# Kernel tuning notes

Measured on AMD Instinct MI355X. Metric: run time of the kernel, lower is better.

## Reference

```python
import jax, jax.numpy as jnp
import numpy as np

N = 100000      # number of edge features (rows of feats)
M = 800000      # number of triplets
HID = 128
HEADS = 8
DH = HID // HEADS


def setup_inputs() -> dict:
    key = jax.random.key(0)
    ks = jax.random.split(key, 10)
    s = 1.0 / np.sqrt(HID)
    inp = {
        "feats": jax.random.normal(ks[0], (N, HID), dtype=jnp.float32),
        "idx_kj": jax.random.randint(ks[1], (M,), 0, N, dtype=jnp.int64),
        "idx_ji": jax.random.randint(ks[2], (M,), 0, N, dtype=jnp.int64),
        "Wv": jax.random.uniform(ks[3], (HID, HID), jnp.float32, -s, s),
        "Wq": jax.random.uniform(ks[4], (HID, HID), jnp.float32, -s, s),
        "Wk": jax.random.uniform(ks[5], (HID, HID), jnp.float32, -s, s),
        "W1": jax.random.uniform(ks[6], (HID, HID), jnp.float32, -s, s),
        "b1": jax.random.uniform(ks[7], (HID,), jnp.float32, -s, s),
        "W2": jax.random.uniform(ks[8], (HID, HID), jnp.float32, -s, s),
        "b2": jax.random.uniform(ks[9], (HID,), jnp.float32, -s, s),
    }
    return inp


def reference(feats, idx_kj, idx_ji, Wv, Wq, Wk, W1, b1, W2, b2):
    # Projections (no bias), reshape to [N, H, Dh]
    v = (feats @ Wv.T).reshape(N, HEADS, DH)
    k = (feats @ Wk.T).reshape(N, HEADS, DH)
    q = (feats @ Wq.T).reshape(N, HEADS, DH)

    # edge-indexed attention scores: [M, H, 1]
    att = jnp.sum(q[idx_kj] * k[idx_ji], axis=-1, keepdims=True)
    att = jnp.exp(jax.nn.leaky_relu(att, negative_slope=0.2))  # unsafe softmax, as in source

    # segment-sum normalizer over destination index idx_ji: [N, H, 1]
    denom = jax.ops.segment_sum(att, idx_ji, num_segments=N)
    att = att / denom[idx_ji]

    # weighted V gather-scatter: [M, HID] -> [N, HID]
    v_att = (v[idx_kj] * att).reshape(M, HID)
    agg = jax.ops.segment_sum(v_att, idx_ji, num_segments=N)  # v_clone after +scatter-v

    v_flat = v.reshape(N, HID)
    # ResidualLayer (dropout in eval mode -> identity): v + relu(lin2(relu(lin1(agg))))
    h = jax.nn.relu(agg @ W1.T + b1)
    h = jax.nn.relu(h @ W2.T + b2)
    return v_flat + h
```

## Files before the change

kernel.cpp:

```cpp
#include <hip/hip_runtime.h>
#include <hip/hip_bf16.h>
#include <math.h>

#define N_NODES 100000
#define M_EDGES 800000
#define HID 128
#define HEADS 8
#define DH 16
#define SCAN_NB ((N_NODES + 1023) / 1024)

typedef __attribute__((ext_vector_type(8))) short short8;
typedef __attribute__((ext_vector_type(4))) float floatx4;

__device__ __forceinline__ ushort f32_to_bf16(float x) {
    __hip_bfloat16 h = __float2bfloat16(x);
    union { __hip_bfloat16 h; ushort u; } c; c.h = h;
    return c.u;
}
__device__ __forceinline__ float bf16_bits_to_f32(ushort u) {
    union { unsigned int i; float f; } c; c.i = ((unsigned int)u) << 16;
    return c.f;
}
__device__ __forceinline__ float bf16pair_lo(unsigned int p) {
    union { unsigned int i; float f; } c; c.i = p << 16; return c.f;
}
__device__ __forceinline__ float bf16pair_hi(unsigned int p) {
    union { unsigned int i; float f; } c; c.i = p & 0xffff0000u; return c.f;
}

__device__ __forceinline__ void stage_w_frag(const ushort* __restrict__ W,
                                             ushort* __restrict__ lds, int tid)
{
    #pragma unroll
    for (int i = 0; i < 8; ++i) {
        int idx  = i * 256 + tid;
        int f    = idx >> 6;
        int lane = idx & 63;
        int t    = f & 7, ks = f >> 3;
        int row  = t * 16 + (lane & 15);
        int col  = ks * 32 + (lane >> 4) * 8;
        uint4 d = *(const uint4*)(W + row * HID + col);
        *(uint4*)(lds + idx * 8) = d;
    }
}

__global__ __launch_bounds__(256) void cvt_w_kernel(
    const float* __restrict__ Wq, const float* __restrict__ Wk, const float* __restrict__ Wv,
    const float* __restrict__ W1, const float* __restrict__ W2,
    ushort* __restrict__ dq, ushort* __restrict__ dk, ushort* __restrict__ dv,
    ushort* __restrict__ d1, ushort* __restrict__ d2)
{
    int i = blockIdx.x * 256 + threadIdx.x;
    int w = i >> 14;
    int j = i & 16383;
    const float* s[5] = {Wq, Wk, Wv, W1, W2};
    ushort*      d[5] = {dq, dk, dv, d1, d2};
    d[w][j] = f32_to_bf16(s[w][j]);
}

__global__ __launch_bounds__(256) void qkv_mfma_kernel(
    const float* __restrict__ feats,
    const ushort* __restrict__ Wq16, const ushort* __restrict__ Wk16, const ushort* __restrict__ Wv16,
    ushort* __restrict__ qv16, ushort* __restrict__ k16)
{
    __shared__ ushort wlds[16384];
    const int tid  = threadIdx.x;
    const int wave = tid >> 6;
    const int lane = tid & 63;
    const int row0 = blockIdx.x * 128 + wave * 32;
    const int lrow = lane & 15;
    const int lk   = (lane >> 4) * 8;
    const int crow = (lane >> 4) * 4;

    short8 afrag[2][4];
    bool tvalid[2];
    #pragma unroll
    for (int r = 0; r < 2; ++r) {
        int rr = row0 + r * 16;
        tvalid[r] = (rr < N_NODES);
        const float* arow = feats + (size_t)((tvalid[r] ? rr : 0) + lrow) * HID + lk;
        #pragma unroll
        for (int ks = 0; ks < 4; ++ks) {
            float4 f0 = *(const float4*)(arow + ks * 32);
            float4 f1 = *(const float4*)(arow + ks * 32 + 4);
            short8 a;
            a[0] = (short)f32_to_bf16(f0.x); a[1] = (short)f32_to_bf16(f0.y);
            a[2] = (short)f32_to_bf16(f0.z); a[3] = (short)f32_to_bf16(f0.w);
            a[4] = (short)f32_to_bf16(f1.x); a[5] = (short)f32_to_bf16(f1.y);
            a[6] = (short)f32_to_bf16(f1.z); a[7] = (short)f32_to_bf16(f1.w);
            afrag[r][ks] = a;
        }
    }

    const ushort* Ws[3] = {Wq16, Wk16, Wv16};
    ushort* Ob[3]; int Ostride[3];
    Ob[0] = qv16;       Ostride[0] = 256;
    Ob[1] = k16;        Ostride[1] = 128;
    Ob[2] = qv16 + 128; Ostride[2] = 256;

    #pragma unroll
    for (int w = 0; w < 3; ++w) {
        __syncthreads();
        stage_w_frag(Ws[w], wlds, tid);
        __syncthreads();

        floatx4 acc[2][8];
        #pragma unroll
        for (int r = 0; r < 2; ++r)
            #pragma unroll
            for (int t = 0; t < 8; ++t) acc[r][t] = (floatx4)(0.f);

        #pragma unroll
        for (int ks = 0; ks < 4; ++ks) {
            short8 B[8];
            #pragma unroll
            for (int t = 0; t < 8; ++t)
                B[t] = *(const short8*)&wlds[(ks * 8 + t) * 512 + lane * 8];
            #pragma unroll
            for (int t = 0; t < 8; ++t) {
                acc[0][t] = __builtin_amdgcn_mfma_f32_16x16x32_bf16(B[t], afrag[0][ks], acc[0][t], 0, 0, 0);
                acc[1][t] = __builtin_amdgcn_mfma_f32_16x16x32_bf16(B[t], afrag[1][ks], acc[1][t], 0, 0, 0);
            }
        }

        #pragma unroll
        for (int r = 0; r < 2; ++r) {
            if (tvalid[r]) {
                ushort* O = Ob[w] + (size_t)(row0 + r * 16 + lrow) * Ostride[w];
                #pragma unroll
                for (int t = 0; t < 8; ++t) {
                    ushort4 o;
                    o.x = f32_to_bf16(acc[r][t][0]); o.y = f32_to_bf16(acc[r][t][1]);
                    o.z = f32_to_bf16(acc[r][t][2]); o.w = f32_to_bf16(acc[r][t][3]);
                    *(ushort4*)(O + t * 16 + crow) = o;
                }
            }
        }
    }
}

__global__ __launch_bounds__(256) void hist_kernel(
    const int* __restrict__ idx_ji, int* __restrict__ count)
{
    int m = blockIdx.x * 256 + threadIdx.x;
    if (m < M_EDGES) atomicAdd(&count[idx_ji[m]], 1);
}

__global__ __launch_bounds__(256) void scan_blocksum_kernel(
    const int* __restrict__ count, int* __restrict__ blocksum)
{
    __shared__ int s[256];
    const int tid = threadIdx.x;
    const int base = blockIdx.x * 1024 + tid * 4;
    int sum = 0;
    if (base + 3 < N_NODES) {
        int4 c = *(const int4*)(count + base);
        sum = c.x + c.y + c.z + c.w;
    } else {
        #pragma unroll
        for (int j = 0; j < 4; ++j) if (base + j < N_NODES) sum += count[base + j];
    }
    s[tid] = sum;
    __syncthreads();
    for (int off = 128; off > 0; off >>= 1) {
        if (tid < off) s[tid] += s[tid + off];
        __syncthreads();
    }
    if (tid == 0) blocksum[blockIdx.x] = s[0];
}

__global__ __launch_bounds__(128) void scan_top_kernel(int* __restrict__ blocksum)
{
    __shared__ int s[128];
    const int t = threadIdx.x;
    int v = (t < SCAN_NB) ? blocksum[t] : 0;
    s[t] = v;
    __syncthreads();
    for (int off = 1; off < 128; off <<= 1) {
        int x = (t >= off) ? s[t - off] : 0;
        __syncthreads();
        s[t] += x;
        __syncthreads();
    }
    if (t < SCAN_NB) blocksum[t] = s[t] - v;
}

__global__ __launch_bounds__(256) void scan_write_kernel(
    const int* __restrict__ count, const int* __restrict__ blocksum,
    int* __restrict__ offsets, int* __restrict__ cursor)
{
    __shared__ int s[256];
    const int tid = threadIdx.x;
    const int base = blockIdx.x * 1024 + tid * 4;
    int c0 = 0, c1 = 0, c2 = 0, c3 = 0;
    if (base + 3 < N_NODES) {
        int4 c = *(const int4*)(count + base);
        c0 = c.x; c1 = c.y; c2 = c.z; c3 = c.w;
    } else {
        if (base     < N_NODES) c0 = count[base];
        if (base + 1 < N_NODES) c1 = count[base + 1];
        if (base + 2 < N_NODES) c2 = count[base + 2];
        if (base + 3 < N_NODES) c3 = count[base + 3];
    }
    const int tsum = c0 + c1 + c2 + c3;
    s[tid] = tsum;
    __syncthreads();
    for (int off = 1; off < 256; off <<= 1) {
        int x = (tid >= off) ? s[tid - off] : 0;
        __syncthreads();
        s[tid] += x;
        __syncthreads();
    }
    int o0 = s[tid] - tsum + blocksum[blockIdx.x];
    int o1 = o0 + c0, o2 = o1 + c1, o3 = o2 + c2;
    if (base + 3 < N_NODES) {
        *(int4*)(offsets + base) = make_int4(o0, o1, o2, o3);
        *(int4*)(cursor  + base) = make_int4(o0, o1, o2, o3);
    } else {
        if (base     < N_NODES) { offsets[base]     = o0; cursor[base]     = o0; }
        if (base + 1 < N_NODES) { offsets[base + 1] = o1; cursor[base + 1] = o1; }
        if (base + 2 < N_NODES) { offsets[base + 2] = o2; cursor[base + 2] = o2; }
        if (base + 3 < N_NODES) { offsets[base + 3] = o3; cursor[base + 3] = o3; }
    }
}

__global__ __launch_bounds__(256) void fill_kernel(
    const int* __restrict__ idx_ji, const int* __restrict__ idx_kj,
    int* __restrict__ cursor, int* __restrict__ edge_kj)
{
    int m = blockIdx.x * 256 + threadIdx.x;
    if (m < M_EDGES) {
        int pos = atomicAdd(&cursor[idx_ji[m]], 1);
        edge_kj[pos] = idx_kj[m];
    }
}

__global__ __launch_bounds__(256) void aggregate_kernel(
    const int* __restrict__ edge_kj, const int* __restrict__ offsets,
    const int* __restrict__ count, const ushort* __restrict__ qv16,
    const ushort* __restrict__ k16, ushort* __restrict__ agg16)
{
    const int gid  = blockIdx.x * 256 + threadIdx.x;
    const int node = gid >> 4;
    const int l16  = threadIdx.x & 15;
    if (node >= N_NODES) return;

    const int deg  = count[node];
    const int base = offsets[node];

    float kn[8];
    {
        uint4 kp = *(const uint4*)(k16 + (size_t)node * HID + l16 * 8);
        const unsigned int* kw = (const unsigned int*)&kp;
        #pragma unroll
        for (int j = 0; j < 4; ++j) {
            kn[2*j]   = bf16pair_lo(kw[j]);
            kn[2*j+1] = bf16pair_hi(kw[j]);
        }
    }

    float acc[8] = {0.f,0.f,0.f,0.f,0.f,0.f,0.f,0.f};
    float d = 0.f;

    int e = 0;
    for (; e + 2 <= deg; e += 2) {
        const int kj0 = edge_kj[base + e];
        const int kj1 = edge_kj[base + e + 1];
        const ushort* r0 = qv16 + (size_t)kj0 * 256 + l16 * 8;
        const ushort* r1 = qv16 + (size_t)kj1 * 256 + l16 * 8;
        uint4 qp0 = *(const uint4*)r0;
        uint4 vp0 = *(const uint4*)(r0 + 128);
        uint4 qp1 = *(const uint4*)r1;
        uint4 vp1 = *(const uint4*)(r1 + 128);

        const unsigned int* q0 = (const unsigned int*)&qp0;
        const unsigned int* q1 = (const unsigned int*)&qp1;
        float p0 = 0.f, p1 = 0.f;
        #pragma unroll
        for (int j = 0; j < 4; ++j) {
            p0 += bf16pair_lo(q0[j]) * kn[2*j] + bf16pair_hi(q0[j]) * kn[2*j+1];
            p1 += bf16pair_lo(q1[j]) * kn[2*j] + bf16pair_hi(q1[j]) * kn[2*j+1];
        }
        p0 += __shfl_xor(p0, 1);
        p1 += __shfl_xor(p1, 1);
        float lr0 = (p0 >= 0.f) ? p0 : 0.2f * p0;
        float lr1 = (p1 >= 0.f) ? p1 : 0.2f * p1;
        float s0 = __expf(lr0);
        float s1 = __expf(lr1);
        d += s0 + s1;
        const unsigned int* v0 = (const unsigned int*)&vp0;
        const unsigned int* v1 = (const unsigned int*)&vp1;
        #pragma unroll
        for (int j = 0; j < 4; ++j) {
            acc[2*j]   += s0 * bf16pair_lo(v0[j]) + s1 * bf16pair_lo(v1[j]);
            acc[2*j+1] += s0 * bf16pair_hi(v0[j]) + s1 * bf16pair_hi(v1[j]);
        }
    }
    if (e < deg) {
        const int kj0 = edge_kj[base + e];
        const ushort* r0 = qv16 + (size_t)kj0 * 256 + l16 * 8;
        uint4 qp0 = *(const uint4*)r0;
        uint4 vp0 = *(const uint4*)(r0 + 128);
        const unsigned int* q0 = (const unsigned int*)&qp0;
        float p0 = 0.f;
        #pragma unroll
        for (int j = 0; j < 4; ++j)
            p0 += bf16pair_lo(q0[j]) * kn[2*j] + bf16pair_hi(q0[j]) * kn[2*j+1];
        p0 += __shfl_xor(p0, 1);
        float lr0 = (p0 >= 0.f) ? p0 : 0.2f * p0;
        float s0 = __expf(lr0);
        d += s0;
        const unsigned int* v0 = (const unsigned int*)&vp0;
        #pragma unroll
        for (int j = 0; j < 4; ++j) {
            acc[2*j]   += s0 * bf16pair_lo(v0[j]);
            acc[2*j+1] += s0 * bf16pair_hi(v0[j]);
        }
    }

    const float inv = (deg > 0) ? 1.f / d : 0.f;
    uint4 o;
    unsigned int* ow = (unsigned int*)&o;
    #pragma unroll
    for (int j = 0; j < 4; ++j)
        ow[j] = (unsigned int)f32_to_bf16(acc[2*j] * inv)
              | ((unsigned int)f32_to_bf16(acc[2*j+1] * inv) << 16);
    *(uint4*)(agg16 + (size_t)node * HID + l16 * 8) = o;
}

__global__ __launch_bounds__(256) void mlp_mfma_kernel(
    const ushort* __restrict__ agg16, const ushort* __restrict__ qv16,
    const ushort* __restrict__ W1_16, const float* __restrict__ b1,
    const ushort* __restrict__ W2_16, const float* __restrict__ b2,
    float* __restrict__ out)
{
    __shared__ ushort wlds[16384];
    __shared__ ushort h1s[16384];
    const int tid  = threadIdx.x;
    const int wave = tid >> 6;
    const int lane = tid & 63;
    const int row0 = blockIdx.x * 128 + wave * 32;
    const int lrow = lane & 15;
    const int lk   = (lane >> 4) * 8;
    const int crow = (lane >> 4) * 4;

    short8 afrag[2][4];
    bool tvalid[2];
    #pragma unroll
    for (int r = 0; r < 2; ++r) {
        int rr = row0 + r * 16;
        tvalid[r] = (rr < N_NODES);
        const ushort* arow = agg16 + (size_t)((tvalid[r] ? rr : 0) + lrow) * HID + lk;
        #pragma unroll
        for (int ks = 0; ks < 4; ++ks)
            afrag[r][ks] = *(const short8*)(arow + ks * 32);
    }

    stage_w_frag(W1_16, wlds, tid);
    __syncthreads();

    {
        floatx4 acc[2][8];
        #pragma unroll
        for (int r = 0; r < 2; ++r)
            #pragma unroll
            for (int t = 0; t < 8; ++t) acc[r][t] = (floatx4)(0.f);
        #pragma unroll
        for (int ks = 0; ks < 4; ++ks) {
            short8 B[8];
            #pragma unroll
            for (int t = 0; t < 8; ++t)
                B[t] = *(const short8*)&wlds[(ks * 8 + t) * 512 + lane * 8];
            #pragma unroll
            for (int t = 0; t < 8; ++t) {
                acc[0][t] = __builtin_amdgcn_mfma_f32_16x16x32_bf16(B[t], afrag[0][ks], acc[0][t], 0, 0, 0);
                acc[1][t] = __builtin_amdgcn_mfma_f32_16x16x32_bf16(B[t], afrag[1][ks], acc[1][t], 0, 0, 0);
            }
        }
        #pragma unroll
        for (int r = 0; r < 2; ++r) {
            ushort* tile = &h1s[(wave * 2 + r) * 2048];
            #pragma unroll
            for (int t = 0; t < 8; ++t) {
                float4 bias = *(const float4*)(b1 + t * 16 + crow);
                ushort4 o;
                o.x = f32_to_bf16(fmaxf(acc[r][t][0] + bias.x, 0.f));
                o.y = f32_to_bf16(fmaxf(acc[r][t][1] + bias.y, 0.f));
                o.z = f32_to_bf16(fmaxf(acc[r][t][2] + bias.z, 0.f));
                o.w = f32_to_bf16(fmaxf(acc[r][t][3] + bias.w, 0.f));
                int ks   = t >> 1;
                int quad = (t & 1) * 2 + (crow >> 3);
                int j0   = crow & 4;
                *(ushort4*)(tile + (ks * 64 + quad * 16 + lrow) * 8 + j0) = o;
            }
        }
    }
    __syncthreads();
    stage_w_frag(W2_16, wlds, tid);
    __syncthreads();

    {
        short8 hfrag[2][4];
        #pragma unroll
        for (int r = 0; r < 2; ++r) {
            const ushort* tile = &h1s[(wave * 2 + r) * 2048];
            #pragma unroll
            for (int ks = 0; ks < 4; ++ks)
                hfrag[r][ks] = *(const short8*)(tile + (ks * 64 + lane) * 8);
        }
        floatx4 acc[2][8];
        #pragma unroll
        for (int r = 0; r < 2; ++r)
            #pragma unroll
            for (int t = 0; t < 8; ++t) acc[r][t] = (floatx4)(0.f);
        #pragma unroll
        for (int ks = 0; ks < 4; ++ks) {
            short8 B[8];
            #pragma unroll
            for (int t = 0; t < 8; ++t)
                B[t] = *(const short8*)&wlds[(ks * 8 + t) * 512 + lane * 8];
            #pragma unroll
            for (int t = 0; t < 8; ++t) {
                acc[0][t] = __builtin_amdgcn_mfma_f32_16x16x32_bf16(B[t], hfrag[0][ks], acc[0][t], 0, 0, 0);
                acc[1][t] = __builtin_amdgcn_mfma_f32_16x16x32_bf16(B[t], hfrag[1][ks], acc[1][t], 0, 0, 0);
            }
        }
        #pragma unroll
        for (int r = 0; r < 2; ++r) {
            if (tvalid[r]) {
                const size_t nrow = (size_t)(row0 + r * 16 + lrow);
                const ushort* vrow = qv16 + nrow * 256 + 128;
                float* orow = out + nrow * HID;
                #pragma unroll
                for (int t = 0; t < 8; ++t) {
                    float4 bias = *(const float4*)(b2 + t * 16 + crow);
                    ushort4 vv = *(const ushort4*)(vrow + t * 16 + crow);
                    float4 o;
                    o.x = bf16_bits_to_f32(vv.x) + fmaxf(acc[r][t][0] + bias.x, 0.f);
                    o.y = bf16_bits_to_f32(vv.y) + fmaxf(acc[r][t][1] + bias.y, 0.f);
                    o.z = bf16_bits_to_f32(vv.z) + fmaxf(acc[r][t][2] + bias.z, 0.f);
                    o.w = bf16_bits_to_f32(vv.w) + fmaxf(acc[r][t][3] + bias.w, 0.f);
                    *(float4*)(orow + t * 16 + crow) = o;
                }
            }
        }
    }
}

extern "C" void kernel_launch(void* const* d_in, const int* in_sizes, int n_in,
                              void* d_out, int out_size, void* d_ws, size_t ws_size,
                              hipStream_t stream) {
    const float* feats  = (const float*)d_in[0];
    const int*   idx_kj = (const int*)d_in[1];
    const int*   idx_ji = (const int*)d_in[2];
    const float* Wv     = (const float*)d_in[3];
    const float* Wq     = (const float*)d_in[4];
    const float* Wk     = (const float*)d_in[5];
    const float* W1     = (const float*)d_in[6];
    const float* b1     = (const float*)d_in[7];
    const float* W2     = (const float*)d_in[8];
    const float* b2     = (const float*)d_in[9];
    float* out = (float*)d_out;

    ushort* qv16    = (ushort*)d_ws;
    ushort* k16     = qv16    + (size_t)N_NODES * 256;
    ushort* agg16   = k16     + (size_t)N_NODES * HID;
    ushort* Wq16    = agg16   + (size_t)N_NODES * HID;
    ushort* Wk16    = Wq16 + HID * HID;
    ushort* Wv16    = Wk16 + HID * HID;
    ushort* W116    = Wv16 + HID * HID;
    ushort* W216    = W116 + HID * HID;
    int* count      = (int*)(W216 + HID * HID);
    int* offsets    = count + N_NODES;
    int* cursor     = offsets + N_NODES;
    int* blocksum   = cursor + N_NODES;
    int* edge_kj    = blocksum + ((SCAN_NB + 3) & ~3);

    hipMemsetAsync(count, 0, N_NODES * sizeof(int), stream);

    cvt_w_kernel<<<(5 * HID * HID + 255) / 256, 256, 0, stream>>>(
        Wq, Wk, Wv, W1, W2, Wq16, Wk16, Wv16, W116, W216);

    qkv_mfma_kernel<<<(N_NODES + 127) / 128, 256, 0, stream>>>(
        feats, Wq16, Wk16, Wv16, qv16, k16);

    hist_kernel<<<(M_EDGES + 255) / 256, 256, 0, stream>>>(idx_ji, count);
    scan_blocksum_kernel<<<SCAN_NB, 256, 0, stream>>>(count, blocksum);
    scan_top_kernel<<<1, 128, 0, stream>>>(blocksum);
    scan_write_kernel<<<SCAN_NB, 256, 0, stream>>>(count, blocksum, offsets, cursor);
    fill_kernel<<<(M_EDGES + 255) / 256, 256, 0, stream>>>(idx_ji, idx_kj, cursor, edge_kj);

    aggregate_kernel<<<((size_t)N_NODES * 16 + 255) / 256, 256, 0, stream>>>(
        edge_kj, offsets, count, qv16, k16, agg16);

    mlp_mfma_kernel<<<(N_NODES + 127) / 128, 256, 0, stream>>>(
        agg16, qv16, W116, b1, W216, b2, out);
}
```

Before: 328.5 us.

## Fold weight conversion, memset and top scan into kernels; pad CSR for vector edge loads

Removes the separate weight-conversion kernel by converting fp32 weights to bf16 while staging them into LDS. The count memset moves into the QKV kernel and the single-block top-level scan is recomputed redundantly in each scan_write block, which removes several launches. Per-node edge lists are padded to multiples of four so the aggregate loop can read four edge indices with one int4 load and issue four gathers per iteration. In exchange it adds redundant fp32 weight loads per block, a larger edge buffer, and wasted lanes on padded edges.

```diff
diff --git a/kernel.cpp b/kernel.cpp
--- a/kernel.cpp
+++ b/kernel.cpp
@@ -28,8 +28,8 @@
     union { unsigned int i; float f; } c; c.i = p & 0xffff0000u; return c.f;
 }
 
-__device__ __forceinline__ void stage_w_frag(const ushort* __restrict__ W,
-                                             ushort* __restrict__ lds, int tid)
+__device__ __forceinline__ void stage_w_frag_f32(const float* __restrict__ W,
+                                                 ushort* __restrict__ lds, int tid)
 {
     #pragma unroll
     for (int i = 0; i < 8; ++i) {
@@ -39,29 +39,23 @@
         int t    = f & 7, ks = f >> 3;
         int row  = t * 16 + (lane & 15);
         int col  = ks * 32 + (lane >> 4) * 8;
-        uint4 d = *(const uint4*)(W + row * HID + col);
-        *(uint4*)(lds + idx * 8) = d;
-    }
-}
-
-__global__ __launch_bounds__(256) void cvt_w_kernel(
-    const float* __restrict__ Wq, const float* __restrict__ Wk, const float* __restrict__ Wv,
-    const float* __restrict__ W1, const float* __restrict__ W2,
-    ushort* __restrict__ dq, ushort* __restrict__ dk, ushort* __restrict__ dv,
-    ushort* __restrict__ d1, ushort* __restrict__ d2)
-{
-    int i = blockIdx.x * 256 + threadIdx.x;
-    int w = i >> 14;
-    int j = i & 16383;
-    const float* s[5] = {Wq, Wk, Wv, W1, W2};
-    ushort*      d[5] = {dq, dk, dv, d1, d2};
-    d[w][j] = f32_to_bf16(s[w][j]);
+        const float* src = W + row * HID + col;
+        float4 a = *(const float4*)src;
+        float4 b = *(const float4*)(src + 4);
+        ushort4 lo, hi;
+        lo.x = f32_to_bf16(a.x); lo.y = f32_to_bf16(a.y);
+        lo.z = f32_to_bf16(a.z); lo.w = f32_to_bf16(a.w);
+        hi.x = f32_to_bf16(b.x); hi.y = f32_to_bf16(b.y);
+        hi.z = f32_to_bf16(b.z); hi.w = f32_to_bf16(b.w);
+        *(ushort4*)(lds + idx * 8)     = lo;
+        *(ushort4*)(lds + idx * 8 + 4) = hi;
+    }
 }
 
 __global__ __launch_bounds__(256) void qkv_mfma_kernel(
     const float* __restrict__ feats,
-    const ushort* __restrict__ Wq16, const ushort* __restrict__ Wk16, const ushort* __restrict__ Wv16,
-    ushort* __restrict__ qv16, ushort* __restrict__ k16)
+    const float* __restrict__ Wq, const float* __restrict__ Wk, const float* __restrict__ Wv,
+    ushort* __restrict__ qv16, ushort* __restrict__ k16, int* __restrict__ count)
 {
     __shared__ ushort wlds[16384];
     const int tid  = threadIdx.x;
@@ -71,6 +65,9 @@
     const int lrow = lane & 15;
     const int lk   = (lane >> 4) * 8;
     const int crow = (lane >> 4) * 4;
+
+    int z = blockIdx.x * 256 + tid;
+    if (z < N_NODES) count[z] = 0;
 
     short8 afrag[2][4];
     bool tvalid[2];
@@ -92,7 +89,7 @@
         }
     }
 
-    const ushort* Ws[3] = {Wq16, Wk16, Wv16};
+    const float* Ws[3] = {Wq, Wk, Wv};
     ushort* Ob[3]; int Ostride[3];
     Ob[0] = qv16;       Ostride[0] = 256;
     Ob[1] = k16;        Ostride[1] = 128;
@@ -101,7 +98,7 @@
     #pragma unroll
     for (int w = 0; w < 3; ++w) {
         __syncthreads();
-        stage_w_frag(Ws[w], wlds, tid);
+        stage_w_frag_f32(Ws[w], wlds, tid);
         __syncthreads();
 
         floatx4 acc[2][8];
@@ -155,10 +152,11 @@
     int sum = 0;
     if (base + 3 < N_NODES) {
         int4 c = *(const int4*)(count + base);
-        sum = c.x + c.y + c.z + c.w;
+        sum = ((c.x + 3) & ~3) + ((c.y + 3) & ~3) + ((c.z + 3) & ~3) + ((c.w + 3) & ~3);
     } else {
         #pragma unroll
-        for (int j = 0; j < 4; ++j) if (base + j < N_NODES) sum += count[base + j];
+        for (int j = 0; j < 4; ++j)
+            if (base + j < N_NODES) sum += (count[base + j] + 3) & ~3;
     }
     s[tid] = sum;
     __syncthreads();
@@ -167,22 +165,6 @@
         __syncthreads();
     }
     if (tid == 0) blocksum[blockIdx.x] = s[0];
-}
-
-__global__ __launch_bounds__(128) void scan_top_kernel(int* __restrict__ blocksum)
-{
-    __shared__ int s[128];
-    const int t = threadIdx.x;
-    int v = (t < SCAN_NB) ? blocksum[t] : 0;
-    s[t] = v;
-    __syncthreads();
-    for (int off = 1; off < 128; off <<= 1) {
-        int x = (t >= off) ? s[t - off] : 0;
-        __syncthreads();
-        s[t] += x;
-        __syncthreads();
-    }
-    if (t < SCAN_NB) blocksum[t] = s[t] - v;
 }
 
 __global__ __launch_bounds__(256) void scan_write_kernel(
@@ -190,17 +172,29 @@
     int* __restrict__ offsets, int* __restrict__ cursor)
 {
     __shared__ int s[256];
+    __shared__ int bs[128];
     const int tid = threadIdx.x;
+
+    if (tid < 128) bs[tid] = (tid < SCAN_NB) ? blocksum[tid] : 0;
+    __syncthreads();
+    for (int off = 1; off < 128; off <<= 1) {
+        int x = (tid >= off && tid < 128) ? bs[tid - off] : 0;
+        __syncthreads();
+        if (tid < 128) bs[tid] += x;
+        __syncthreads();
+    }
+    const int blockbase = (blockIdx.x == 0) ? 0 : bs[blockIdx.x - 1];
+
     const int base = blockIdx.x * 1024 + tid * 4;
     int c0 = 0, c1 = 0, c2 = 0, c3 = 0;
     if (base + 3 < N_NODES) {
         int4 c = *(const int4*)(count + base);
-        c0 = c.x; c1 = c.y; c2 = c.z; c3 = c.w;
+        c0 = (c.x + 3) & ~3; c1 = (c.y + 3) & ~3; c2 = (c.z + 3) & ~3; c3 = (c.w + 3) & ~3;
     } else {
-        if (base     < N_NODES) c0 = count[base];
-        if (base + 1 < N_NODES) c1 = count[base + 1];
-        if (base + 2 < N_NODES) c2 = count[base + 2];
-        if (base + 3 < N_NODES) c3 = count[base + 3];
+        if (base     < N_NODES) c0 = (count[base]     + 3) & ~3;
+        if (base + 1 < N_NODES) c1 = (count[base + 1] + 3) & ~3;
+        if (base + 2 < N_NODES) c2 = (count[base + 2] + 3) & ~3;
+        if (base + 3 < N_NODES) c3 = (count[base + 3] + 3) & ~3;
     }
     const int tsum = c0 + c1 + c2 + c3;
     s[tid] = tsum;
@@ -211,7 +205,7 @@
         s[tid] += x;
         __syncthreads();
     }
-    int o0 = s[tid] - tsum + blocksum[blockIdx.x];
+    int o0 = s[tid] - tsum + blockbase;
     int o1 = o0 + c0, o2 = o1 + c1, o3 = o2 + c2;
     if (base + 3 < N_NODES) {
         *(int4*)(offsets + base) = make_int4(o0, o1, o2, o3);
@@ -262,59 +256,47 @@
     float acc[8] = {0.f,0.f,0.f,0.f,0.f,0.f,0.f,0.f};
     float d = 0.f;
 
-    int e = 0;
-    for (; e + 2 <= deg; e += 2) {
-        const int kj0 = edge_kj[base + e];
-        const int kj1 = edge_kj[base + e + 1];
-        const ushort* r0 = qv16 + (size_t)kj0 * 256 + l16 * 8;
-        const ushort* r1 = qv16 + (size_t)kj1 * 256 + l16 * 8;
-        uint4 qp0 = *(const uint4*)r0;
-        uint4 vp0 = *(const uint4*)(r0 + 128);
-        uint4 qp1 = *(const uint4*)r1;
-        uint4 vp1 = *(const uint4*)(r1 + 128);
-
-        const unsigned int* q0 = (const unsigned int*)&qp0;
-        const unsigned int* q1 = (const unsigned int*)&qp1;
-        float p0 = 0.f, p1 = 0.f;
-        #pragma unroll
-        for (int j = 0; j < 4; ++j) {
-            p0 += bf16pair_lo(q0[j]) * kn[2*j] + bf16pair_hi(q0[j]) * kn[2*j+1];
-            p1 += bf16pair_lo(q1[j]) * kn[2*j] + bf16pair_hi(q1[j]) * kn[2*j+1];
-        }
-        p0 += __shfl_xor(p0, 1);
-        p1 += __shfl_xor(p1, 1);
-        float lr0 = (p0 >= 0.f) ? p0 : 0.2f * p0;
-        float lr1 = (p1 >= 0.f) ? p1 : 0.2f * p1;
-        float s0 = __expf(lr0);
-        float s1 = __expf(lr1);
-        d += s0 + s1;
-        const unsigned int* v0 = (const unsigned int*)&vp0;
-        const unsigned int* v1 = (const unsigned int*)&vp1;
-        #pragma unroll
-        for (int j = 0; j < 4; ++j) {
-            acc[2*j]   += s0 * bf16pair_lo(v0[j]) + s1 * bf16pair_lo(v1[j]);
-            acc[2*j+1] += s0 * bf16pair_hi(v0[j]) + s1 * bf16pair_hi(v1[j]);
-        }
-    }
-    if (e < deg) {
-        const int kj0 = edge_kj[base + e];
-        const ushort* r0 = qv16 + (size_t)kj0 * 256 + l16 * 8;
-        uint4 qp0 = *(const uint4*)r0;
-        uint4 vp0 = *(const uint4*)(r0 + 128);
-        const unsigned int* q0 = (const unsigned int*)&qp0;
-        float p0 = 0.f;
-        #pragma unroll
-        for (int j = 0; j < 4; ++j)
-            p0 += bf16pair_lo(q0[j]) * kn[2*j] + bf16pair_hi(q0[j]) * kn[2*j+1];
-        p0 += __shfl_xor(p0, 1);
-        float lr0 = (p0 >= 0.f) ? p0 : 0.2f * p0;
-        float s0 = __expf(lr0);
-        d += s0;
-        const unsigned int* v0 = (const unsigned int*)&vp0;
-        #pragma unroll
-        for (int j = 0; j < 4; ++j) {
-            acc[2*j]   += s0 * bf16pair_lo(v0[j]);
-            acc[2*j+1] += s0 * bf16pair_hi(v0[j]);
+    for (int e = 0; e < deg; e += 4) {
+        const int rem = deg - e;
+        int4 kj4 = *(const int4*)(edge_kj + base + e);
+        int kj[4];
+        kj[0] = kj4.x;
+        kj[1] = (rem > 1) ? kj4.y : kj4.x;
+        kj[2] = (rem > 2) ? kj4.z : kj4.x;
+        kj[3] = (rem > 3) ? kj4.w : kj4.x;
+
+        uint4 qp[4], vp[4];
+        #pragma unroll
+        for (int i = 0; i < 4; ++i) {
+            const ushort* r = qv16 + (size_t)kj[i] * 256 + l16 * 8;
+            qp[i] = *(const uint4*)r;
+            vp[i] = *(const uint4*)(r + 128);
+        }
+
+        float p[4];
+        #pragma unroll
+        for (int i = 0; i < 4; ++i) {
+            const unsigned int* q = (const unsigned int*)&qp[i];
+            float x = 0.f;
+            #pragma unroll
+            for (int j = 0; j < 4; ++j)
+                x += bf16pair_lo(q[j]) * kn[2*j] + bf16pair_hi(q[j]) * kn[2*j+1];
+            p[i] = x;
+        }
+        #pragma unroll
+        for (int i = 0; i < 4; ++i) p[i] += __shfl_xor(p[i], 1);
+
+        #pragma unroll
+        for (int i = 0; i < 4; ++i) {
+            float lr = (p[i] >= 0.f) ? p[i] : 0.2f * p[i];
+            float s  = (i < rem) ? __expf(lr) : 0.f;
+            d += s;
+            const unsigned int* v = (const unsigned int*)&vp[i];
+            #pragma unroll
+            for (int j = 0; j < 4; ++j) {
+                acc[2*j]   += s * bf16pair_lo(v[j]);
+                acc[2*j+1] += s * bf16pair_hi(v[j]);
+            }
         }
     }
 
@@ -330,8 +312,8 @@
 
 __global__ __launch_bounds__(256) void mlp_mfma_kernel(
     const ushort* __restrict__ agg16, const ushort* __restrict__ qv16,
-    const ushort* __restrict__ W1_16, const float* __restrict__ b1,
-    const ushort* __restrict__ W2_16, const float* __restrict__ b2,
+    const float* __restrict__ W1, const float* __restrict__ b1,
+    const float* __restrict__ W2, const float* __restrict__ b2,
     float* __restrict__ out)
 {
     __shared__ ushort wlds[16384];
@@ -356,7 +338,7 @@
             afrag[r][ks] = *(const short8*)(arow + ks * 32);
     }
 
-    stage_w_frag(W1_16, wlds, tid);
+    stage_w_frag_f32(W1, wlds, tid);
     __syncthreads();
 
     {
@@ -396,7 +378,7 @@
         }
     }
     __syncthreads();
-    stage_w_frag(W2_16, wlds, tid);
+    stage_w_frag_f32(W2, wlds, tid);
     __syncthreads();
 
     {
@@ -465,28 +447,17 @@
     ushort* qv16    = (ushort*)d_ws;
     ushort* k16     = qv16    + (size_t)N_NODES * 256;
     ushort* agg16   = k16     + (size_t)N_NODES * HID;
-    ushort* Wq16    = agg16   + (size_t)N_NODES * HID;
-    ushort* Wk16    = Wq16 + HID * HID;
-    ushort* Wv16    = Wk16 + HID * HID;
-    ushort* W116    = Wv16 + HID * HID;
-    ushort* W216    = W116 + HID * HID;
-    int* count      = (int*)(W216 + HID * HID);
+    int* count      = (int*)(agg16 + (size_t)N_NODES * HID);
     int* offsets    = count + N_NODES;
     int* cursor     = offsets + N_NODES;
     int* blocksum   = cursor + N_NODES;
-    int* edge_kj    = blocksum + ((SCAN_NB + 3) & ~3);
-
-    hipMemsetAsync(count, 0, N_NODES * sizeof(int), stream);
-
-    cvt_w_kernel<<<(5 * HID * HID + 255) / 256, 256, 0, stream>>>(
-        Wq, Wk, Wv, W1, W2, Wq16, Wk16, Wv16, W116, W216);
+    int* edge_kj    = blocksum + 128;
 
     qkv_mfma_kernel<<<(N_NODES + 127) / 128, 256, 0, stream>>>(
-        feats, Wq16, Wk16, Wv16, qv16, k16);
+        feats, Wq, Wk, Wv, qv16, k16, count);
 
     hist_kernel<<<(M_EDGES + 255) / 256, 256, 0, stream>>>(idx_ji, count);
     scan_blocksum_kernel<<<SCAN_NB, 256, 0, stream>>>(count, blocksum);
-    scan_top_kernel<<<1, 128, 0, stream>>>(blocksum);
     scan_write_kernel<<<SCAN_NB, 256, 0, stream>>>(count, blocksum, offsets, cursor);
     fill_kernel<<<(M_EDGES + 255) / 256, 256, 0, stream>>>(idx_ji, idx_kj, cursor, edge_kj);
 
@@ -494,5 +465,5 @@
         edge_kj, offsets, count, qv16, k16, agg16);
 
     mlp_mfma_kernel<<<(N_NODES + 127) / 128, 256, 0, stream>>>(
-        agg16, qv16, W116, b1, W216, b2, out);
-}
+        agg16, qv16, W1, b1, W2, b2, out);
+}
```

Measured after the change: 334.7 us. About the same (+1.9%).
